# Kernel tuning notes

Measured on AMD Instinct MI355X. Metric: run time of the kernel, lower is better.

The kernel has to match this reference:

```python
import jax, jax.numpy as jnp
import numpy as np

# Model dims (match init_kwargs defaults)
H, DK, DV = 6, 256, 512          # num_heads, head_k_dim, head_v_dim (= head_dim*expand_v)
HID = 2048                       # hidden_size
CONV = 4                         # short conv kernel size
NORM_EPS = 1e-5


def causal_dwconv_silu(x, w):
    """Depthwise causal conv1d (kernel CONV) + SiLU. x: [B,T,C], w: [C,K]."""
    K = w.shape[1]
    xp = jnp.pad(x, ((0, 0), (K - 1, 0), (0, 0)))
    y = jax.lax.conv_general_dilated(
        jnp.transpose(xp, (0, 2, 1)),            # [B,C,T+K-1]
        w[:, None, :],                            # [C,1,K] depthwise
        (1,), 'VALID', feature_group_count=w.shape[0])
    return jax.nn.silu(jnp.transpose(y, (0, 2, 1)))  # [B,T,C]


def l2norm(x, eps=1e-6):
    return x * jax.lax.rsqrt(jnp.sum(x * x, axis=-1, keepdims=True) + eps)


def setup_inputs() -> dict:
    key = jax.random.key(0)
    ks = jax.random.split(key, 16)
    B, T = 2, 4096
    s = HID ** -0.5
    return dict(
        hidden_states=jax.random.normal(ks[0], (B, T, HID), jnp.float32),
        Wq=jax.random.normal(ks[1], (H * DK, HID), jnp.float32) * s,
        Wk=jax.random.normal(ks[2], (H * DK, HID), jnp.float32) * s,
        Wv=jax.random.normal(ks[3], (H * DV, HID), jnp.float32) * s,
        Wb=jax.random.normal(ks[4], (H, HID), jnp.float32) * s,
        Wa=jax.random.normal(ks[5], (H, HID), jnp.float32) * s,
        A_log=jnp.log(jax.random.uniform(ks[6], (H,), jnp.float32, 0.5, 16.0)),
        dt_bias=jax.random.normal(ks[7], (H,), jnp.float32) * 0.1,
        conv_wq=jax.random.normal(ks[8], (H * DK, CONV), jnp.float32) * 0.5,
        conv_wk=jax.random.normal(ks[9], (H * DK, CONV), jnp.float32) * 0.5,
        conv_wv=jax.random.normal(ks[10], (H * DV, CONV), jnp.float32) * 0.5,
        Wg=jax.random.normal(ks[11], (H * DV, HID), jnp.float32) * s,
        norm_w=jnp.ones((DV,), jnp.float32),
        Wo=jax.random.normal(ks[12], (HID, H * DV), jnp.float32) * (H * DV) ** -0.5,
    )


def reference(hidden_states, Wq, Wk, Wv, Wb, Wa, A_log, dt_bias,
              conv_wq, conv_wk, conv_wv, Wg, norm_w, Wo):
    x = hidden_states
    B, T, _ = x.shape
    # projections + short conv + SiLU
    q = causal_dwconv_silu(x @ Wq.T, conv_wq).reshape(B, T, H, DK)
    k = causal_dwconv_silu(x @ Wk.T, conv_wk).reshape(B, T, H, DK)
    v = causal_dwconv_silu(x @ Wv.T, conv_wv).reshape(B, T, H, DV)
    beta = jax.nn.sigmoid(x @ Wb.T)                                   # [B,T,H]
    g = -jnp.exp(A_log) * jax.nn.softplus(x @ Wa.T + dt_bias)        # [B,T,H] (log decay)
    # qk l2-norm + scale, as in gated delta rule kernels
    q = l2norm(q) * (DK ** -0.5)
    k = l2norm(k)

    # gated delta rule recurrence: S_t = exp(g_t)*S_{t-1} + beta_t * k_t (v_t - k_t^T exp(g_t) S_{t-1})
    def step(S, inp):
        qt, kt, vt, gt, bt = inp  # [B,H,DK],[B,H,DK],[B,H,DV],[B,H],[B,H]
        S = S * jnp.exp(gt)[..., None, None]                  # [B,H,DK,DV]
        v_new = vt - jnp.einsum('bhk,bhkv->bhv', kt, S)
        S = S + bt[..., None, None] * (kt[..., :, None] * v_new[..., None, :])
        o = jnp.einsum('bhk,bhkv->bhv', qt, S)
        return S, o

    S0 = jnp.zeros((B, H, DK, DV), x.dtype)
    tm = lambda a: jnp.moveaxis(a, 1, 0)  # time-major for scan
    _, o = jax.lax.scan(step, S0, (tm(q), tm(k), tm(v), tm(g), tm(beta)))
    o = jnp.moveaxis(o, 0, 1)  # [B,T,H,DV]

    # per-head RMSNorm (fp32 var) then SiLU output gate
    var = jnp.mean(jnp.square(o.astype(jnp.float32)), axis=-1, keepdims=True)
    o = o * jax.lax.rsqrt(var + NORM_EPS).astype(o.dtype) * norm_w
    gate = (x @ Wg.T).reshape(B, T, H, DV)
    o = o * jax.nn.silu(gate)
    return o.reshape(B, T, H * DV) @ Wo.T
```

## Files before the change

kernel.cpp:

```cpp
#include <hip/hip_runtime.h>
#include <hip/hip_bf16.h>
#include <math.h>

#define NH 6
#define DKk 256
#define DVv 512
#define HIDDIM 2048
#define TT 4096
#define NBb 2
#define MTOK (NBb*TT)
#define CH 64
#define NCH (TT/CH)
#define SCLN 136

typedef __hip_bfloat16 bf16;
typedef __attribute__((ext_vector_type(8))) short bf16x8;
typedef __attribute__((ext_vector_type(4))) float f32x4;

union FragU { bf16x8 v; uint2 u2[2]; uint4 u4; };
union BfBits { bf16 h; unsigned short s; };
union U4S8 { uint4 u; unsigned short s[8]; };

__device__ inline float bflo(unsigned u) { return __uint_as_float(u << 16); }
__device__ inline float bfhi(unsigned u) { return __uint_as_float(u & 0xffff0000u); }
__device__ inline unsigned short bfbits(float f) {
    BfBits b; b.h = __float2bfloat16(f); return b.s;
}
__device__ inline float bf2f(unsigned short s) { return __uint_as_float(((unsigned)s) << 16); }
__device__ inline uint4 pack8(float4 a, float4 b) {
    U4S8 r;
    r.s[0] = bfbits(a.x); r.s[1] = bfbits(a.y); r.s[2] = bfbits(a.z); r.s[3] = bfbits(a.w);
    r.s[4] = bfbits(b.x); r.s[5] = bfbits(b.y); r.s[6] = bfbits(b.z); r.s[7] = bfbits(b.w);
    return r.u;
}
__device__ inline uint2 packh4(float a, float b, float c, float d) {
    union { unsigned short s[4]; uint2 u; } r;
    r.s[0] = bfbits(a); r.s[1] = bfbits(b); r.s[2] = bfbits(c); r.s[3] = bfbits(d);
    return r.u;
}
__device__ inline bf16x8 pk8t(f32x4 a, f32x4 b) {
    U4S8 r;
    r.s[0] = bfbits(a[0]); r.s[1] = bfbits(a[1]); r.s[2] = bfbits(a[2]); r.s[3] = bfbits(a[3]);
    r.s[4] = bfbits(b[0]); r.s[5] = bfbits(b[1]); r.s[6] = bfbits(b[2]); r.s[7] = bfbits(b[3]);
    FragU f; f.u4 = r.u; return f.v;
}

typedef const __attribute__((address_space(1))) void* gas_ptr;
typedef __attribute__((address_space(3))) void* las_ptr;
__device__ inline void gld16(const void* g, void* s) {
    __builtin_amdgcn_global_load_lds((gas_ptr)g, (las_ptr)s, 16, 0, 0);
}

__device__ inline bf16x8 lfrag256(const short* sh, int n0, int k0) {
    int lane = threadIdx.x & 63;
    int r = n0 + (lane & 15);
    int c = k0 + ((lane >> 4) * 4);
    FragU f;
    f.u2[0] = *(const uint2*)((const char*)sh + (((r * 256 + c) * 2) ^ ((r & 7) << 4)));
    f.u2[1] = *(const uint2*)((const char*)sh + (((r * 256 + c + 16) * 2) ^ ((r & 7) << 4)));
    return f.v;
}
__device__ inline bf16x8 lfrag64(const short* sh, int n0, int k0) {
    int lane = threadIdx.x & 63;
    int r = n0 + (lane & 15);
    int c = k0 + ((lane >> 4) * 4);
    FragU f;
    f.u2[0] = *(const uint2*)((const char*)sh + (((r * 64 + c) * 2) ^ ((r & 7) << 4)));
    f.u2[1] = *(const uint2*)((const char*)sh + (((r * 64 + c + 16) * 2) ^ ((r & 7) << 4)));
    return f.v;
}
__device__ inline bf16x8 lfrag72(const short* sh, int n0, int k0) {
    int lane = threadIdx.x & 63;
    int r = n0 + (lane & 15);
    int c = k0 + ((lane >> 4) * 4);
    FragU f;
    f.u2[0] = *(const uint2*)((const char*)sh + (r * 72 + c) * 2);
    f.u2[1] = *(const uint2*)((const char*)sh + (r * 72 + c + 16) * 2);
    return f.v;
}
__device__ inline bf16x8 mfrag(const float* Msh, const float* colscale, int m0, int k0) {
    int lane = threadIdx.x & 63;
    int t = m0 + (lane & 15);
    int s0 = k0 + ((lane >> 4) * 4);
    U4S8 r;
#pragma unroll
    for (int i = 0; i < 4; ++i) {
        r.s[i]     = bfbits(Msh[t * 68 + s0 + i]      * colscale[s0 + i]);
        r.s[4 + i] = bfbits(Msh[t * 68 + s0 + 16 + i] * colscale[s0 + 16 + i]);
    }
    FragU f; f.u4 = r.u; return f.v;
}

__global__ __launch_bounds__(256) void cvt_bf16(const float* __restrict__ in,
                                                bf16* __restrict__ out, int n) {
    for (int i = (blockIdx.x * 256 + threadIdx.x) * 4; i < n; i += gridDim.x * 256 * 4) {
        float4 v = *(const float4*)(in + i);
        *(uint2*)(out + i) = packh4(v.x, v.y, v.z, v.w);
    }
}

template <typename TC>
__global__ __launch_bounds__(256) void mfma_gemm_bb(const bf16* __restrict__ A,
                                                    const bf16* __restrict__ B,
                                                    TC* __restrict__ C,
                                                    int M, int N, int K) {
    __shared__ __align__(16) short As[128 * 64];
    __shared__ __align__(16) short Bs[128 * 64];
    const int tid = threadIdx.x;
    const int lane = tid & 63;
    const int wid = tid >> 6;
    const int wr = wid >> 1, wc = wid & 1;
    const int bm = blockIdx.y * 128, bn = blockIdx.x * 128;

    f32x4 acc[4][4];
#pragma unroll
    for (int i = 0; i < 4; ++i)
#pragma unroll
        for (int j = 0; j < 4; ++j) acc[i][j] = f32x4{0.f, 0.f, 0.f, 0.f};

    for (int k0 = 0; k0 < K; k0 += 64) {
        __syncthreads();
#pragma unroll
        for (int i = 0; i < 4; ++i) {
            int r0 = wid * 32 + i * 8;
            const bf16* ga = A + (size_t)(bm + r0 + (lane >> 3)) * K + k0 + (lane & 7) * 8;
            const bf16* gb = B + (size_t)(bn + r0 + (lane >> 3)) * K + k0 + (lane & 7) * 8;
            gld16(ga, &As[r0 * 64]);
            gld16(gb, &Bs[r0 * 64]);
        }
        __syncthreads();
#pragma unroll
        for (int kk = 0; kk < 2; ++kk) {
            bf16x8 af[4], bfr[4];
#pragma unroll
            for (int i = 0; i < 4; ++i) {
                FragU f;
                f.u4 = *(const uint4*)&As[(wr * 64 + i * 16 + (lane & 15)) * 64 +
                                          kk * 32 + (lane >> 4) * 8];
                af[i] = f.v;
            }
#pragma unroll
            for (int j = 0; j < 4; ++j) {
                FragU f;
                f.u4 = *(const uint4*)&Bs[(wc * 64 + j * 16 + (lane & 15)) * 64 +
                                          kk * 32 + (lane >> 4) * 8];
                bfr[j] = f.v;
            }
#pragma unroll
            for (int i = 0; i < 4; ++i)
#pragma unroll
                for (int j = 0; j < 4; ++j)
                    acc[i][j] = __builtin_amdgcn_mfma_f32_16x16x32_bf16(
                        af[i], bfr[j], acc[i][j], 0, 0, 0);
        }
    }
#pragma unroll
    for (int i = 0; i < 4; ++i)
#pragma unroll
        for (int j = 0; j < 4; ++j) {
            int row = bm + wr * 64 + i * 16 + (lane >> 4) * 4;
            int col = bn + wc * 64 + j * 16 + (lane & 15);
#pragma unroll
            for (int qi = 0; qi < 4; ++qi) {
                float vv = acc[i][j][qi];
                if constexpr (sizeof(TC) == 2)
                    C[(size_t)(row + qi) * N + col] = __float2bfloat16(vv);
                else
                    C[(size_t)(row + qi) * N + col] = vv;
            }
        }
}

template <typename TA, typename TC>
__global__ __launch_bounds__(256) void mfma_gemm_nt(const TA* __restrict__ A,
                                                    const float* __restrict__ B,
                                                    TC* __restrict__ C,
                                                    int M, int N, int K) {
    __shared__ __align__(16) short As[128 * 64];
    __shared__ __align__(16) short Bs[128 * 64];
    const int tid = threadIdx.x;
    const int lane = tid & 63;
    const int wid = tid >> 6;
    const int wr = wid >> 1, wc = wid & 1;
    const int bm = blockIdx.y * 128, bn = blockIdx.x * 128;
    const int srow = tid >> 1;
    const int sks = (tid & 1) * 32;

    f32x4 acc[4][4];
#pragma unroll
    for (int i = 0; i < 4; ++i)
#pragma unroll
        for (int j = 0; j < 4; ++j) acc[i][j] = f32x4{0.f, 0.f, 0.f, 0.f};

    auto swzb = [](int row, int kelem) {
        return ((row * 64 + kelem) * 2) ^ ((row & 7) << 4);
    };
    uint4 ra[4], rb[4];
    auto fetch = [&](int k0) {
        if constexpr (sizeof(TA) == 2) {
            const uint4* pa = (const uint4*)(A + (size_t)(bm + srow) * K + k0 + sks);
#pragma unroll
            for (int j = 0; j < 4; ++j) ra[j] = pa[j];
        } else {
            const float4* pa = (const float4*)(A + (size_t)(bm + srow) * K + k0 + sks);
#pragma unroll
            for (int j = 0; j < 4; ++j) ra[j] = pack8(pa[2 * j], pa[2 * j + 1]);
        }
        const float4* pb = (const float4*)(B + (size_t)(bn + srow) * K + k0 + sks);
#pragma unroll
        for (int j = 0; j < 4; ++j) rb[j] = pack8(pb[2 * j], pb[2 * j + 1]);
    };
    auto store_lds = [&]() {
#pragma unroll
        for (int j = 0; j < 4; ++j) {
            int byte = swzb(srow, sks + 8 * j);
            *(uint4*)((char*)As + byte) = ra[j];
            *(uint4*)((char*)Bs + byte) = rb[j];
        }
    };
    auto rdfrag = [&](const short* Sm, int row, int kbase) {
        FragU f;
        int ko = kbase + (lane >> 4) * 4;
        f.u2[0] = *(const uint2*)((const char*)Sm + swzb(row, ko));
        f.u2[1] = *(const uint2*)((const char*)Sm + swzb(row, ko + 16));
        return f.v;
    };

    fetch(0);
    for (int k0 = 0; k0 < K; k0 += 64) {
        __syncthreads();
        store_lds();
        __syncthreads();
        if (k0 + 64 < K) fetch(k0 + 64);
#pragma unroll
        for (int kk = 0; kk < 2; ++kk) {
            bf16x8 af[4], bfr[4];
#pragma unroll
            for (int i = 0; i < 4; ++i)
                af[i] = rdfrag(As, wr * 64 + i * 16 + (lane & 15), kk * 32);
#pragma unroll
            for (int j = 0; j < 4; ++j)
                bfr[j] = rdfrag(Bs, wc * 64 + j * 16 + (lane & 15), kk * 32);
#pragma unroll
            for (int i = 0; i < 4; ++i)
#pragma unroll
                for (int j = 0; j < 4; ++j)
                    acc[i][j] = __builtin_amdgcn_mfma_f32_16x16x32_bf16(
                        af[i], bfr[j], acc[i][j], 0, 0, 0);
        }
    }
#pragma unroll
    for (int i = 0; i < 4; ++i)
#pragma unroll
        for (int j = 0; j < 4; ++j) {
            int row = bm + wr * 64 + i * 16 + (lane >> 4) * 4;
            int col = bn + wc * 64 + j * 16 + (lane & 15);
#pragma unroll
            for (int qi = 0; qi < 4; ++qi) {
                float vv = acc[i][j][qi];
                if constexpr (sizeof(TC) == 2)
                    C[(size_t)(row + qi) * N + col] = __float2bfloat16(vv);
                else
                    C[(size_t)(row + qi) * N + col] = vv;
            }
        }
}

__global__ __launch_bounds__(256) void convnorm_qk(const bf16* __restrict__ pre,
                                                   const float* __restrict__ cw,
                                                   bf16* __restrict__ out,
                                                   float scale) {
    const int bth = blockIdx.x;
    const int h = bth % NH;
    const int bt = bth / NH;
    const int t = bt % TT;
    const int d = threadIdx.x;
    const int c = h * DKk + d;
    const int C = NH * DKk;
    const bf16* p = pre + (size_t)bt * C + c;

    float w0 = cw[c * 4 + 0], w1 = cw[c * 4 + 1], w2 = cw[c * 4 + 2], w3 = cw[c * 4 + 3];
    float y = w3 * __bfloat162float(p[0]);
    if (t >= 1) y = fmaf(w2, __bfloat162float(p[-(ptrdiff_t)C]), y);
    if (t >= 2) y = fmaf(w1, __bfloat162float(p[-(ptrdiff_t)(2 * C)]), y);
    if (t >= 3) y = fmaf(w0, __bfloat162float(p[-(ptrdiff_t)(3 * C)]), y);
    y = y / (1.f + expf(-y));

    float s = y * y;
#pragma unroll
    for (int off = 32; off >= 1; off >>= 1) s += __shfl_down(s, off, 64);
    __shared__ float red[4];
    if ((threadIdx.x & 63) == 0) red[threadIdx.x >> 6] = s;
    __syncthreads();
    float tot = (red[0] + red[1]) + (red[2] + red[3]);
    out[(size_t)bt * C + c] = __float2bfloat16(y * rsqrtf(tot + 1e-6f) * scale);
}

__global__ __launch_bounds__(256) void conv_v_kernel(const bf16* __restrict__ pre,
                                                     const float* __restrict__ cw,
                                                     bf16* __restrict__ out) {
    const int C = NH * DVv;
    int idx = blockIdx.x * 256 + threadIdx.x;
    int c = idx % C;
    int bt = idx / C;
    int t = bt % TT;
    const bf16* p = pre + (size_t)bt * C + c;
    float y = cw[c * 4 + 3] * __bfloat162float(p[0]);
    if (t >= 1) y = fmaf(cw[c * 4 + 2], __bfloat162float(p[-(ptrdiff_t)C]), y);
    if (t >= 2) y = fmaf(cw[c * 4 + 1], __bfloat162float(p[-(ptrdiff_t)(2 * C)]), y);
    if (t >= 3) y = fmaf(cw[c * 4 + 0], __bfloat162float(p[-(ptrdiff_t)(3 * C)]), y);
    out[(size_t)bt * C + c] = __float2bfloat16(y / (1.f + expf(-y)));
}

__global__ __launch_bounds__(256) void proj_ab(const float* __restrict__ x,
                                               const float* __restrict__ Wb,
                                               const float* __restrict__ Wa,
                                               const float* __restrict__ A_log,
                                               const float* __restrict__ dt_bias,
                                               float* __restrict__ beta,
                                               float* __restrict__ g) {
    const int bt = blockIdx.x;
    const int tid = threadIdx.x;
    const float* xr = x + (size_t)bt * HIDDIM;
    float accb[NH], acca[NH];
#pragma unroll
    for (int h = 0; h < NH; ++h) { accb[h] = 0.f; acca[h] = 0.f; }
    for (int k0 = tid; k0 < HIDDIM; k0 += 256) {
        float xv = xr[k0];
#pragma unroll
        for (int h = 0; h < NH; ++h) {
            accb[h] = fmaf(xv, Wb[h * HIDDIM + k0], accb[h]);
            acca[h] = fmaf(xv, Wa[h * HIDDIM + k0], acca[h]);
        }
    }
#pragma unroll
    for (int h = 0; h < NH; ++h) {
#pragma unroll
        for (int off = 32; off >= 1; off >>= 1) {
            accb[h] += __shfl_down(accb[h], off, 64);
            acca[h] += __shfl_down(acca[h], off, 64);
        }
    }
    __shared__ float redb[NH][4], reda[NH][4];
    int wv = tid >> 6;
    if ((tid & 63) == 0) {
#pragma unroll
        for (int h = 0; h < NH; ++h) { redb[h][wv] = accb[h]; reda[h][wv] = acca[h]; }
    }
    __syncthreads();
    if (tid < NH) {
        float sb = (redb[tid][0] + redb[tid][1]) + (redb[tid][2] + redb[tid][3]);
        float sa = (reda[tid][0] + reda[tid][1]) + (reda[tid][2] + reda[tid][3]);
        beta[(size_t)bt * NH + tid] = 1.f / (1.f + expf(-sb));
        float xg = sa + dt_bias[tid];
        float sp = fmaxf(xg, 0.f) + log1pf(expf(-fabsf(xg)));
        g[(size_t)bt * NH + tid] = -expf(A_log[tid]) * sp;
    }
}

__global__ __launch_bounds__(256) void chunk_prep(const bf16* __restrict__ qbuf,
                                                  const bf16* __restrict__ kbuf,
                                                  bf16* __restrict__ vbuf,
                                                  bf16* __restrict__ tvbuf,
                                                  const float* __restrict__ gbuf,
                                                  const float* __restrict__ bbuf,
                                                  bf16* __restrict__ Bmat,
                                                  float* __restrict__ scl) {
    __shared__ __align__(16) short Ksh[64 * 256];
    __shared__ __align__(16) short Qsh[64 * 256];
    __shared__ __align__(16) float Ash[64 * 68];
    __shared__ __align__(16) short Vt[128 * 72];
    __shared__ float Lsh[64], betash[64], lamsh[64], blamsh[64];

    const int blk = blockIdx.x;
    const int c = blk % NCH;
    const int hh = (blk / NCH) % NH;
    const int b = blk / (NCH * NH);
    const int tid = threadIdx.x;
    const int wid = tid >> 6;
    const int lane = tid & 63;
    const int bt0 = b * TT + c * CH;
    const int cid = (b * NH + hh) * NCH + c;

    {
        int r = tid >> 2, c0 = (tid & 3) * 64;
        const uint4* kg = (const uint4*)(kbuf + (size_t)(bt0 + r) * 1536 + hh * 256 + c0);
        const uint4* qg = (const uint4*)(qbuf + (size_t)(bt0 + r) * 1536 + hh * 256 + c0);
#pragma unroll
        for (int j = 0; j < 8; ++j) {
            int byte = ((r * 256 + c0 + j * 8) * 2) ^ ((r & 7) << 4);
            *(uint4*)((char*)Ksh + byte) = kg[j];
            *(uint4*)((char*)Qsh + byte) = qg[j];
        }
    }
    if (tid < 64) {
        float gv = gbuf[(size_t)(bt0 + tid) * NH + hh];
        float bv = bbuf[(size_t)(bt0 + tid) * NH + hh];
        float L = gv;
#pragma unroll
        for (int off = 1; off < 64; off <<= 1) {
            float o = __shfl_up(L, off, 64);
            if (lane >= off) L += o;
        }
        float L63 = __shfl(L, 63, 64);
        float lam = expf(L);
        Lsh[tid] = L; betash[tid] = bv; lamsh[tid] = lam; blamsh[tid] = bv * lam;
        scl[(size_t)cid * SCLN + tid] = expf(L63 - L);
        scl[(size_t)cid * SCLN + 68 + tid] = lam;
        if (tid == 63) scl[(size_t)cid * SCLN + 64] = lam;
    }
    __syncthreads();

    f32x4 akk[4], aqk[4];
#pragma unroll
    for (int n = 0; n < 4; ++n) { akk[n] = f32x4{0,0,0,0}; aqk[n] = f32x4{0,0,0,0}; }
#pragma unroll
    for (int kk = 0; kk < 8; ++kk) {
        bf16x8 aK = lfrag256(Ksh, wid * 16, kk * 32);
        bf16x8 aQ = lfrag256(Qsh, wid * 16, kk * 32);
#pragma unroll
        for (int n = 0; n < 4; ++n) {
            bf16x8 bK = lfrag256(Ksh, n * 16, kk * 32);
            akk[n] = __builtin_amdgcn_mfma_f32_16x16x32_bf16(aK, bK, akk[n], 0, 0, 0);
            aqk[n] = __builtin_amdgcn_mfma_f32_16x16x32_bf16(aQ, bK, aqk[n], 0, 0, 0);
        }
    }
#pragma unroll
    for (int n = 0; n < 4; ++n)
#pragma unroll
        for (int qi = 0; qi < 4; ++qi) {
            int i = wid * 16 + (lane >> 4) * 4 + qi;
            int s = n * 16 + (lane & 15);
            float av = 0.f, bvv = 0.f;
            if (s <= i) {
                float sc2 = expf(Lsh[i] - Lsh[s]);
                if (s < i) av = betash[i] * sc2 * akk[n][qi];
                bvv = sc2 * aqk[n][qi];
            }
            Ash[i * 68 + s] = av;
            Bmat[(size_t)cid * 4096 + i * 64 + s] = __float2bfloat16(bvv);
        }
    __syncthreads();

    if (wid == 0) {
        float mm[64];
        mm[0] = (lane == 0) ? 1.f : 0.f;
#pragma unroll
        for (int t = 1; t < 64; ++t) {
            float a0 = 0.f, a1 = 0.f, a2 = 0.f, a3 = 0.f;
#pragma unroll
            for (int s = 0; s < t; ++s) {
                float Av = Ash[t * 68 + s];
                if ((s & 3) == 0) a0 = fmaf(Av, mm[s], a0);
                else if ((s & 3) == 1) a1 = fmaf(Av, mm[s], a1);
                else if ((s & 3) == 2) a2 = fmaf(Av, mm[s], a2);
                else a3 = fmaf(Av, mm[s], a3);
            }
            mm[t] = ((t == lane) ? 1.f : 0.f) - ((a0 + a1) + (a2 + a3));
        }
#pragma unroll
        for (int t = 0; t < 64; ++t) Ash[t * 68 + lane] = mm[t];
    }
    __syncthreads();

    for (int q = 0; q < 4; ++q) {
        {
            int i = tid >> 2, d0 = (tid & 3) * 32;
            const uint4* vg = (const uint4*)(vbuf + (size_t)(bt0 + i) * 3072 + hh * 512 + q * 128 + d0);
#pragma unroll
            for (int jb = 0; jb < 4; ++jb) {
                U4S8 u; u.u = vg[jb];
#pragma unroll
                for (int e = 0; e < 8; ++e)
                    Vt[(d0 + jb * 8 + e) * 72 + i] = (short)u.s[e];
            }
        }
        __syncthreads();
        f32x4 acc[8];
#pragma unroll
        for (int n = 0; n < 8; ++n) acc[n] = f32x4{0,0,0,0};
#pragma unroll
        for (int kk = 0; kk < 2; ++kk) {
            bf16x8 am = mfrag(Ash, betash, wid * 16, kk * 32);
#pragma unroll
            for (int n = 0; n < 8; ++n) {
                bf16x8 bv8 = lfrag72(Vt, n * 16, kk * 32);
                acc[n] = __builtin_amdgcn_mfma_f32_16x16x32_bf16(am, bv8, acc[n], 0, 0, 0);
            }
        }
#pragma unroll
        for (int n = 0; n < 8; ++n)
#pragma unroll
            for (int qi = 0; qi < 4; ++qi) {
                int t = wid * 16 + (lane >> 4) * 4 + qi;
                int d = q * 128 + n * 16 + (lane & 15);
                tvbuf[(size_t)(bt0 + t) * 3072 + hh * 512 + d] = __float2bfloat16(acc[n][qi]);
            }
        __syncthreads();
    }

    {
        int j = tid;
        unsigned short rowv[64];
#pragma unroll
        for (int s = 0; s < 64; ++s)
            rowv[s] = *(const unsigned short*)((const char*)Ksh + (((s * 256 + j) * 2) ^ ((s & 7) << 4)));
#pragma unroll
        for (int sb = 0; sb < 8; ++sb) {
            U4S8 u;
#pragma unroll
            for (int e = 0; e < 8; ++e) u.s[e] = rowv[sb * 8 + e];
            *(uint4*)((char*)Qsh + (((j * 64 + sb * 8) * 2) ^ ((j & 7) << 4))) = u.u;
        }
    }
    __syncthreads();

    {
        f32x4 acc[16];
#pragma unroll
        for (int n = 0; n < 16; ++n) acc[n] = f32x4{0,0,0,0};
#pragma unroll
        for (int kk = 0; kk < 2; ++kk) {
            bf16x8 am = mfrag(Ash, blamsh, wid * 16, kk * 32);
#pragma unroll
            for (int n = 0; n < 16; ++n) {
                bf16x8 bk = lfrag64(Qsh, n * 16, kk * 32);
                acc[n] = __builtin_amdgcn_mfma_f32_16x16x32_bf16(am, bk, acc[n], 0, 0, 0);
            }
        }
#pragma unroll
        for (int n = 0; n < 16; ++n)
#pragma unroll
            for (int qi = 0; qi < 4; ++qi) {
                int t = wid * 16 + (lane >> 4) * 4 + qi;
                int j = n * 16 + (lane & 15);
                vbuf[(size_t)(bt0 + t) * 3072 + hh * 512 + j] = __float2bfloat16(acc[n][qi]);
            }
    }
    {
        int j = tid;
#pragma unroll
        for (int sb = 0; sb < 8; ++sb) {
            uint4 u = *(uint4*)((char*)Qsh + (((j * 64 + sb * 8) * 2) ^ ((j & 7) << 4)));
            *(uint4*)(vbuf + (size_t)(bt0 + (j >> 2)) * 3072 + hh * 512 + 256 + (j & 3) * 64 + sb * 8) = u;
        }
    }
}

__global__ __launch_bounds__(512, 1) void chunk_scan3(const bf16* __restrict__ qbuf,
                                                      const bf16* __restrict__ vbuf,
                                                      bf16* __restrict__ tvbuf,
                                                      const bf16* __restrict__ Bmat,
                                                      const float* __restrict__ scl) {
    __shared__ __align__(16) short TkL[64 * 256];
    __shared__ __align__(16) short QL[64 * 256];
    __shared__ __align__(16) short KTL[256 * 64];
    __shared__ __align__(16) short BmL[64 * 64];
    const int tid = threadIdx.x;
    const int wid = tid >> 6;
    const int lane = tid & 63;
    const int part = blockIdx.x & 3;
    const int bh = blockIdx.x >> 2;
    const int hh = bh % NH;
    const int b = bh / NH;
    const int slice = part * 8 + wid;
    const int dglob0 = hh * 512 + slice * 16;
    const int tlo = (lane >> 4) * 4;
    const int dcol = lane & 15;

    f32x4 S[16];
#pragma unroll
    for (int i = 0; i < 16; ++i) S[i] = f32x4{0.f, 0.f, 0.f, 0.f};

    for (int c = 0; c < NCH; ++c) {
        const int bt0 = b * TT + c * CH;
        const int cid = (b * NH + hh) * NCH + c;
        const float* sc = scl + (size_t)cid * SCLN;
        const float lamC = sc[64];

        __syncthreads();
        {
            int r = tid >> 3;
            int bc0 = (tid & 7) * 16;
#pragma unroll
            for (int rd = 0; rd < 4; ++rd) {
                int bc = bc0 + rd * 128;
                uint4 tv = *(const uint4*)((const char*)(vbuf) +
                    ((size_t)(bt0 + r) * 3072 + hh * 512) * 2 + bc);
                uint4 qv = *(const uint4*)((const char*)(qbuf) +
                    ((size_t)(bt0 + r) * 1536 + hh * 256) * 2 + bc);
                int byte = (r * 512 + bc) ^ ((r & 7) << 4);
                *(uint4*)((char*)TkL + byte) = tv;
                *(uint4*)((char*)QL + byte) = qv;
            }
        }
        {
            int j = tid >> 1;
            int bc0 = (tid & 1) * 16;
#pragma unroll
            for (int rd = 0; rd < 4; ++rd) {
                int bc = bc0 + rd * 32;
                uint4 v = *(const uint4*)((const char*)(vbuf) +
                    ((size_t)(bt0 + (j >> 2)) * 3072 + hh * 512 + 256 + (j & 3) * 64) * 2 + bc);
                int byte = (j * 128 + bc) ^ ((j & 7) << 4);
                *(uint4*)((char*)KTL + byte) = v;
            }
        }
        {
            int r = tid >> 3;
            int bc = (tid & 7) * 16;
            uint4 v = *(const uint4*)((const char*)(Bmat) +
                ((size_t)cid * 4096 + r * 64) * 2 + bc);
            int byte = (r * 128 + bc) ^ ((r & 7) << 4);
            *(uint4*)((char*)BmL + byte) = v;
        }
        __syncthreads();

        bf16x8 sfr[8];
#pragma unroll
        for (int kk = 0; kk < 8; ++kk) sfr[kk] = pk8t(S[2 * kk], S[2 * kk + 1]);

        f32x4 P[4], O[4];
#pragma unroll
        for (int tf = 0; tf < 4; ++tf) { P[tf] = f32x4{0,0,0,0}; O[tf] = f32x4{0,0,0,0}; }
#pragma unroll
        for (int tf = 0; tf < 4; ++tf)
#pragma unroll
            for (int kk = 0; kk < 8; ++kk) {
                bf16x8 aT = lfrag256(TkL, tf * 16, kk * 32);
                bf16x8 aQ = lfrag256(QL, tf * 16, kk * 32);
                P[tf] = __builtin_amdgcn_mfma_f32_16x16x32_bf16(aT, sfr[kk], P[tf], 0, 0, 0);
                O[tf] = __builtin_amdgcn_mfma_f32_16x16x32_bf16(aQ, sfr[kk], O[tf], 0, 0, 0);
            }
#pragma unroll
        for (int tf = 0; tf < 4; ++tf) {
            float4 lam4 = *(const float4*)(sc + 68 + tf * 16 + tlo);
            O[tf][0] *= lam4.x; O[tf][1] *= lam4.y; O[tf][2] *= lam4.z; O[tf][3] *= lam4.w;
            int t = tf * 16 + tlo;
#pragma unroll
            for (int qi = 0; qi < 4; ++qi) {
                float tv = __bfloat162float(tvbuf[(size_t)(bt0 + t + qi) * 3072 + dglob0 + dcol]);
                P[tf][qi] = tv - P[tf][qi];
            }
        }
        bf16x8 ufr0 = pk8t(P[0], P[1]);
        bf16x8 ufr1 = pk8t(P[2], P[3]);
#pragma unroll
        for (int tf = 0; tf < 4; ++tf) {
            bf16x8 aB0 = lfrag64(BmL, tf * 16, 0);
            bf16x8 aB1 = lfrag64(BmL, tf * 16, 32);
            O[tf] = __builtin_amdgcn_mfma_f32_16x16x32_bf16(aB0, ufr0, O[tf], 0, 0, 0);
            O[tf] = __builtin_amdgcn_mfma_f32_16x16x32_bf16(aB1, ufr1, O[tf], 0, 0, 0);
            int t = tf * 16 + tlo;
#pragma unroll
            for (int qi = 0; qi < 4; ++qi)
                tvbuf[(size_t)(bt0 + t + qi) * 3072 + dglob0 + dcol] = __float2bfloat16(O[tf][qi]);
        }
        bf16x8 utfr[2];
#pragma unroll
        for (int k2 = 0; k2 < 2; ++k2) {
            float4 e0 = *(const float4*)(sc + k2 * 32 + tlo);
            float4 e1 = *(const float4*)(sc + k2 * 32 + 16 + tlo);
            f32x4 ua = P[2 * k2], ub = P[2 * k2 + 1];
            ua[0] *= e0.x; ua[1] *= e0.y; ua[2] *= e0.z; ua[3] *= e0.w;
            ub[0] *= e1.x; ub[1] *= e1.y; ub[2] *= e1.z; ub[3] *= e1.w;
            utfr[k2] = pk8t(ua, ub);
        }
#pragma unroll
        for (int kt = 0; kt < 16; ++kt) {
            S[kt][0] *= lamC; S[kt][1] *= lamC; S[kt][2] *= lamC; S[kt][3] *= lamC;
        }
#pragma unroll
        for (int kt = 0; kt < 16; ++kt)
#pragma unroll
            for (int k2 = 0; k2 < 2; ++k2) {
                bf16x8 aK = lfrag64(KTL, kt * 16, k2 * 32);
                S[kt] = __builtin_amdgcn_mfma_f32_16x16x32_bf16(aK, utfr[k2], S[kt], 0, 0, 0);
            }
    }
}

__global__ __launch_bounds__(256) void rmsgate_kernel(bf16* __restrict__ o,
                                                      const bf16* __restrict__ gate,
                                                      const float* __restrict__ norm_w) {
    const int bhead = blockIdx.x;
    const int d = threadIdx.x;
    bf16* op = o + (size_t)bhead * DVv;
    const bf16* gp = gate + (size_t)bhead * DVv;
    float x0 = __bfloat162float(op[d]), x1 = __bfloat162float(op[d + 256]);
    float s = x0 * x0 + x1 * x1;
#pragma unroll
    for (int off = 32; off >= 1; off >>= 1) s += __shfl_down(s, off, 64);
    __shared__ float red[4];
    if ((threadIdx.x & 63) == 0) red[threadIdx.x >> 6] = s;
    __syncthreads();
    float tot = (red[0] + red[1]) + (red[2] + red[3]);
    float r = rsqrtf(tot * (1.f / DVv) + 1e-5f);
    float g0 = __bfloat162float(gp[d]), g1 = __bfloat162float(gp[d + 256]);
    g0 = g0 / (1.f + expf(-g0));
    g1 = g1 / (1.f + expf(-g1));
    op[d]       = __float2bfloat16(x0 * r * norm_w[d] * g0);
    op[d + 256] = __float2bfloat16(x1 * r * norm_w[d + 256] * g1);
}

__global__ void fill_kernel(float* p, int n, float v) {
    int i = blockIdx.x * 256 + threadIdx.x;
    if (i < n) p[i] = v;
}

extern "C" void kernel_launch(void* const* d_in, const int* in_sizes, int n_in,
                              void* d_out, int out_size, void* d_ws, size_t ws_size,
                              hipStream_t stream) {
    const float* x       = (const float*)d_in[0];
    const float* Wq      = (const float*)d_in[1];
    const float* Wk      = (const float*)d_in[2];
    const float* Wv      = (const float*)d_in[3];
    const float* Wb      = (const float*)d_in[4];
    const float* Wa      = (const float*)d_in[5];
    const float* A_log   = (const float*)d_in[6];
    const float* dt_bias = (const float*)d_in[7];
    const float* cwq     = (const float*)d_in[8];
    const float* cwk     = (const float*)d_in[9];
    const float* cwv     = (const float*)d_in[10];
    const float* Wg      = (const float*)d_in[11];
    const float* norm_w  = (const float*)d_in[12];
    const float* Wo      = (const float*)d_in[13];
    float* out = (float*)d_out;

    bf16* qb = (bf16*)d_out;
    bf16* kb = qb + (size_t)MTOK * 1536;

    const size_t elemsA = (size_t)MTOK * 3072;
    const size_t elemsB = (size_t)MTOK * 3072;
    bf16* wsA   = (bf16*)d_ws;
    bf16* wsB   = wsA + elemsA;
    bf16* Bmat  = wsB + elemsB;
    float* scl  = (float*)(Bmat + (size_t)NBb * NH * NCH * 4096);
    float* betab = scl + (size_t)NBb * NH * NCH * SCLN;
    float* gb    = betab + (size_t)MTOK * NH;
    size_t need_base = ((size_t)(gb - (float*)d_ws) + (size_t)MTOK * NH) * sizeof(float);
    bf16* xb    = (bf16*)(gb + (size_t)MTOK * NH);
    bf16* Wslot = xb + (size_t)MTOK * HIDDIM;
    size_t need_fast = need_base +
        ((size_t)MTOK * HIDDIM + (size_t)3072 * HIDDIM) * sizeof(bf16);

    if (ws_size < need_base) {
        fill_kernel<<<(out_size + 255) / 256, 256, 0, stream>>>(out, out_size, 1e9f);
        return;
    }

    dim3 blk(256);
    const bool fast = (ws_size >= need_fast);

    if (fast) {
        cvt_bf16<<<2048, blk, 0, stream>>>(x, xb, MTOK * HIDDIM);
        cvt_bf16<<<1024, blk, 0, stream>>>(Wq, Wslot, 1536 * HIDDIM);
        mfma_gemm_bb<bf16><<<dim3(12, 64), blk, 0, stream>>>(xb, Wslot, wsA, MTOK, 1536, HIDDIM);
        convnorm_qk<<<MTOK * NH, dim3(DKk), 0, stream>>>(wsA, cwq, qb, 0.0625f);
        cvt_bf16<<<1024, blk, 0, stream>>>(Wk, Wslot, 1536 * HIDDIM);
        mfma_gemm_bb<bf16><<<dim3(12, 64), blk, 0, stream>>>(xb, Wslot, wsA, MTOK, 1536, HIDDIM);
        convnorm_qk<<<MTOK * NH, dim3(DKk), 0, stream>>>(wsA, cwk, kb, 1.0f);
        cvt_bf16<<<2048, blk, 0, stream>>>(Wv, Wslot, 3072 * HIDDIM);
        mfma_gemm_bb<bf16><<<dim3(24, 64), blk, 0, stream>>>(xb, Wslot, wsB, MTOK, 3072, HIDDIM);
        conv_v_kernel<<<(MTOK * 3072) / 256, blk, 0, stream>>>(wsB, cwv, wsA);
        proj_ab<<<MTOK, blk, 0, stream>>>(x, Wb, Wa, A_log, dt_bias, betab, gb);
        chunk_prep<<<NBb * NH * NCH, blk, 0, stream>>>(qb, kb, wsA, wsB, gb, betab, Bmat, scl);
        chunk_scan3<<<NBb * NH * 4, dim3(512), 0, stream>>>(qb, wsA, wsB, Bmat, scl);
        cvt_bf16<<<2048, blk, 0, stream>>>(Wg, Wslot, 3072 * HIDDIM);
        mfma_gemm_bb<bf16><<<dim3(24, 64), blk, 0, stream>>>(xb, Wslot, wsA, MTOK, 3072, HIDDIM);
        rmsgate_kernel<<<MTOK * NH, blk, 0, stream>>>(wsB, wsA, norm_w);
        cvt_bf16<<<2048, blk, 0, stream>>>(Wo, Wslot, 2048 * 3072);
        mfma_gemm_bb<float><<<dim3(16, 64), blk, 0, stream>>>(wsB, Wslot, out, MTOK, 2048, 3072);
    } else {
        mfma_gemm_nt<float, bf16><<<dim3(12, 64), blk, 0, stream>>>(x, Wq, wsA, MTOK, 1536, HIDDIM);
        convnorm_qk<<<MTOK * NH, dim3(DKk), 0, stream>>>(wsA, cwq, qb, 0.0625f);
        mfma_gemm_nt<float, bf16><<<dim3(12, 64), blk, 0, stream>>>(x, Wk, wsA, MTOK, 1536, HIDDIM);
        convnorm_qk<<<MTOK * NH, dim3(DKk), 0, stream>>>(wsA, cwk, kb, 1.0f);
        mfma_gemm_nt<float, bf16><<<dim3(24, 64), blk, 0, stream>>>(x, Wv, wsB, MTOK, 3072, HIDDIM);
        conv_v_kernel<<<(MTOK * 3072) / 256, blk, 0, stream>>>(wsB, cwv, wsA);
        proj_ab<<<MTOK, blk, 0, stream>>>(x, Wb, Wa, A_log, dt_bias, betab, gb);
        chunk_prep<<<NBb * NH * NCH, blk, 0, stream>>>(qb, kb, wsA, wsB, gb, betab, Bmat, scl);
        chunk_scan3<<<NBb * NH * 4, dim3(512), 0, stream>>>(qb, wsA, wsB, Bmat, scl);
        mfma_gemm_nt<float, bf16><<<dim3(24, 64), blk, 0, stream>>>(x, Wg, wsA, MTOK, 3072, HIDDIM);
        rmsgate_kernel<<<MTOK * NH, blk, 0, stream>>>(wsB, wsA, norm_w);
        mfma_gemm_nt<bf16, float><<<dim3(16, 64), blk, 0, stream>>>(wsB, Wo, out, MTOK, 2048, 3072);
    }
}
```

Baseline: 1.848 ms.

## Merge chunk-scan work into two 1024-thread blocks per batch-head

The chunked delta-rule scan now runs as two 1024-thread blocks per (batch, head), each owning 16 value-column slices, instead of four 512-thread blocks with 8 slices each. Each block still loads the shared per-chunk tiles (T/k, q, k-transposed and the B matrix), so this halves the redundant global-to-LDS staging per head, with 1024 threads cooperating on every load. In exchange the grid shrinks from 48 to 24 blocks, barriers span 16 waves, and the launch bound of 1024 threads halves the registers available per wave. That could cause the 64-register state accumulator to spill.

```diff
diff --git a/kernel.cpp b/kernel.cpp
--- a/kernel.cpp
+++ b/kernel.cpp
@@ -547,11 +547,11 @@
     }
 }
 
-__global__ __launch_bounds__(512, 1) void chunk_scan3(const bf16* __restrict__ qbuf,
-                                                      const bf16* __restrict__ vbuf,
-                                                      bf16* __restrict__ tvbuf,
-                                                      const bf16* __restrict__ Bmat,
-                                                      const float* __restrict__ scl) {
+__global__ __launch_bounds__(1024, 4) void chunk_scan6(const bf16* __restrict__ qbuf,
+                                                       const bf16* __restrict__ vbuf,
+                                                       bf16* __restrict__ tvbuf,
+                                                       const bf16* __restrict__ Bmat,
+                                                       const float* __restrict__ scl) {
     __shared__ __align__(16) short TkL[64 * 256];
     __shared__ __align__(16) short QL[64 * 256];
     __shared__ __align__(16) short KTL[256 * 64];
@@ -559,11 +559,11 @@
     const int tid = threadIdx.x;
     const int wid = tid >> 6;
     const int lane = tid & 63;
-    const int part = blockIdx.x & 3;
-    const int bh = blockIdx.x >> 2;
+    const int half = blockIdx.x & 1;
+    const int bh = blockIdx.x >> 1;
     const int hh = bh % NH;
     const int b = bh / NH;
-    const int slice = part * 8 + wid;
+    const int slice = half * 16 + wid;
     const int dglob0 = hh * 512 + slice * 16;
     const int tlo = (lane >> 4) * 4;
     const int dcol = lane & 15;
@@ -579,34 +579,30 @@
         const float lamC = sc[64];
 
         __syncthreads();
-        {
-            int r = tid >> 3;
-            int bc0 = (tid & 7) * 16;
-#pragma unroll
-            for (int rd = 0; rd < 4; ++rd) {
-                int bc = bc0 + rd * 128;
-                uint4 tv = *(const uint4*)((const char*)(vbuf) +
-                    ((size_t)(bt0 + r) * 3072 + hh * 512) * 2 + bc);
-                uint4 qv = *(const uint4*)((const char*)(qbuf) +
-                    ((size_t)(bt0 + r) * 1536 + hh * 256) * 2 + bc);
-                int byte = (r * 512 + bc) ^ ((r & 7) << 4);
-                *(uint4*)((char*)TkL + byte) = tv;
-                *(uint4*)((char*)QL + byte) = qv;
-            }
-        }
-        {
-            int j = tid >> 1;
-            int bc0 = (tid & 1) * 16;
-#pragma unroll
-            for (int rd = 0; rd < 4; ++rd) {
-                int bc = bc0 + rd * 32;
-                uint4 v = *(const uint4*)((const char*)(vbuf) +
-                    ((size_t)(bt0 + (j >> 2)) * 3072 + hh * 512 + 256 + (j & 3) * 64) * 2 + bc);
-                int byte = (j * 128 + bc) ^ ((j & 7) << 4);
-                *(uint4*)((char*)KTL + byte) = v;
-            }
-        }
-        {
+#pragma unroll
+        for (int it = 0; it < 2; ++it) {
+            int u = it * 1024 + tid;
+            int r = u >> 5;
+            int bc = (u & 31) * 16;
+            uint4 tv = *(const uint4*)((const char*)(vbuf) +
+                ((size_t)(bt0 + r) * 3072 + hh * 512) * 2 + bc);
+            uint4 qv = *(const uint4*)((const char*)(qbuf) +
+                ((size_t)(bt0 + r) * 1536 + hh * 256) * 2 + bc);
+            int byte = (r * 512 + bc) ^ ((r & 7) << 4);
+            *(uint4*)((char*)TkL + byte) = tv;
+            *(uint4*)((char*)QL + byte) = qv;
+        }
+#pragma unroll
+        for (int it = 0; it < 2; ++it) {
+            int u = it * 1024 + tid;
+            int j = u >> 3;
+            int bc = (u & 7) * 16;
+            uint4 v = *(const uint4*)((const char*)(vbuf) +
+                ((size_t)(bt0 + (j >> 2)) * 3072 + hh * 512 + 256 + (j & 3) * 64) * 2 + bc);
+            int byte = (j * 128 + bc) ^ ((j & 7) << 4);
+            *(uint4*)((char*)KTL + byte) = v;
+        }
+        if (tid < 512) {
             int r = tid >> 3;
             int bc = (tid & 7) * 16;
             uint4 v = *(const uint4*)((const char*)(Bmat) +
@@ -765,7 +761,7 @@
         conv_v_kernel<<<(MTOK * 3072) / 256, blk, 0, stream>>>(wsB, cwv, wsA);
         proj_ab<<<MTOK, blk, 0, stream>>>(x, Wb, Wa, A_log, dt_bias, betab, gb);
         chunk_prep<<<NBb * NH * NCH, blk, 0, stream>>>(qb, kb, wsA, wsB, gb, betab, Bmat, scl);
-        chunk_scan3<<<NBb * NH * 4, dim3(512), 0, stream>>>(qb, wsA, wsB, Bmat, scl);
+        chunk_scan6<<<NBb * NH * 2, dim3(1024), 0, stream>>>(qb, wsA, wsB, Bmat, scl);
         cvt_bf16<<<2048, blk, 0, stream>>>(Wg, Wslot, 3072 * HIDDIM);
         mfma_gemm_bb<bf16><<<dim3(24, 64), blk, 0, stream>>>(xb, Wslot, wsA, MTOK, 3072, HIDDIM);
         rmsgate_kernel<<<MTOK * NH, blk, 0, stream>>>(wsB, wsA, norm_w);
@@ -780,7 +776,7 @@
         conv_v_kernel<<<(MTOK * 3072) / 256, blk, 0, stream>>>(wsB, cwv, wsA);
         proj_ab<<<MTOK, blk, 0, stream>>>(x, Wb, Wa, A_log, dt_bias, betab, gb);
         chunk_prep<<<NBb * NH * NCH, blk, 0, stream>>>(qb, kb, wsA, wsB, gb, betab, Bmat, scl);
-        chunk_scan3<<<NBb * NH * 4, dim3(512), 0, stream>>>(qb, wsA, wsB, Bmat, scl);
+        chunk_scan6<<<NBb * NH * 2, dim3(1024), 0, stream>>>(qb, wsA, wsB, Bmat, scl);
         mfma_gemm_nt<float, bf16><<<dim3(24, 64), blk, 0, stream>>>(x, Wg, wsA, MTOK, 3072, HIDDIM);
         rmsgate_kernel<<<MTOK * NH, blk, 0, stream>>>(wsB, wsA, norm_w);
         mfma_gemm_nt<bf16, float><<<dim3(16, 64), blk, 0, stream>>>(wsB, Wo, out, MTOK, 2048, 3072);
```

New measurement: 2.573 ms. 39.2% more time.

## Double-buffer chunk scan staging with async global-to-LDS loads

Applied to the files above, without the earlier changes.

The sequential chunk-scan kernel now prefetches the next chunk's Tk and Q tiles into a double-buffered LDS region using global_load_lds, so the loads overlap with the current chunk's MFMA work. The KT tile is staged asynchronously too. The B matrix fragments are read straight from global memory instead of through LDS. The aim is to hide the per-chunk global load latency on the serial critical path, at the cost of more LDS and reordered barriers, with some risk of a synchronization hazard on the KT buffer.

```diff
diff --git a/kernel.cpp b/kernel.cpp
--- a/kernel.cpp
+++ b/kernel.cpp
@@ -51,6 +51,12 @@
     __builtin_amdgcn_global_load_lds((gas_ptr)g, (las_ptr)s, 16, 0, 0);
 }
 
+__device__ inline bf16x8 gfrag(const bf16* base, size_t stride, int n0, int k0) {
+    int lane = threadIdx.x & 63;
+    const bf16* p = base + (size_t)(n0 + (lane & 15)) * stride + k0 + ((lane >> 4) * 4);
+    FragU f; f.u2[0] = *(const uint2*)p; f.u2[1] = *(const uint2*)(p + 16);
+    return f.v;
+}
 __device__ inline bf16x8 lfrag256(const short* sh, int n0, int k0) {
     int lane = threadIdx.x & 63;
     int r = n0 + (lane & 15);
@@ -58,6 +64,15 @@
     FragU f;
     f.u2[0] = *(const uint2*)((const char*)sh + (((r * 256 + c) * 2) ^ ((r & 7) << 4)));
     f.u2[1] = *(const uint2*)((const char*)sh + (((r * 256 + c + 16) * 2) ^ ((r & 7) << 4)));
+    return f.v;
+}
+__device__ inline bf16x8 lfrag512(const short* sh, int n0, int k0, int cofs) {
+    int lane = threadIdx.x & 63;
+    int r = n0 + (lane & 15);
+    int c = cofs + k0 + ((lane >> 4) * 4);
+    FragU f;
+    f.u2[0] = *(const uint2*)((const char*)sh + (((r * 512 + c) * 2) ^ ((r & 7) << 4)));
+    f.u2[1] = *(const uint2*)((const char*)sh + (((r * 512 + c + 16) * 2) ^ ((r & 7) << 4)));
     return f.v;
 }
 __device__ inline bf16x8 lfrag64(const short* sh, int n0, int k0) {
@@ -547,15 +562,13 @@
     }
 }
 
-__global__ __launch_bounds__(512, 1) void chunk_scan3(const bf16* __restrict__ qbuf,
+__global__ __launch_bounds__(512, 1) void chunk_scan7(const bf16* __restrict__ qbuf,
                                                       const bf16* __restrict__ vbuf,
                                                       bf16* __restrict__ tvbuf,
                                                       const bf16* __restrict__ Bmat,
                                                       const float* __restrict__ scl) {
-    __shared__ __align__(16) short TkL[64 * 256];
-    __shared__ __align__(16) short QL[64 * 256];
+    __shared__ __align__(16) short TQ[2][64 * 512];
     __shared__ __align__(16) short KTL[256 * 64];
-    __shared__ __align__(16) short BmL[64 * 64];
     const int tid = threadIdx.x;
     const int wid = tid >> 6;
     const int lane = tid & 63;
@@ -568,53 +581,52 @@
     const int tlo = (lane >> 4) * 4;
     const int dcol = lane & 15;
 
+    auto stage_TkQ = [&](int c2, int bufi) {
+        if (c2 < NCH) {
+            const int bt = b * TT + c2 * CH;
+            short* dst = TQ[bufi];
+#pragma unroll
+            for (int i = 0; i < 8; ++i) {
+                int r = wid * 8 + i;
+                int u = lane ^ (r & 7);
+                const char* src;
+                if (u < 32)
+                    src = (const char*)(vbuf + (size_t)(bt + r) * 3072 + hh * 512) + u * 16;
+                else
+                    src = (const char*)(qbuf + (size_t)(bt + r) * 1536 + hh * 256) + (u - 32) * 16;
+                gld16(src, &dst[r * 512]);
+            }
+        }
+    };
+    auto stage_KT = [&](int c2) {
+        const int bt = b * TT + c2 * CH;
+#pragma unroll
+        for (int i = 0; i < 4; ++i) {
+            int j0 = (wid * 4 + i) * 8;
+            int j = j0 + (lane >> 3);
+            int u = (lane & 7) ^ (j & 7);
+            const char* src = (const char*)(vbuf + (size_t)(bt + (j >> 2)) * 3072 +
+                                            hh * 512 + 256 + (j & 3) * 64) + u * 16;
+            gld16(src, &KTL[j0 * 64]);
+        }
+    };
+
     f32x4 S[16];
 #pragma unroll
     for (int i = 0; i < 16; ++i) S[i] = f32x4{0.f, 0.f, 0.f, 0.f};
+
+    stage_TkQ(0, 0);
+    __syncthreads();
 
     for (int c = 0; c < NCH; ++c) {
         const int bt0 = b * TT + c * CH;
         const int cid = (b * NH + hh) * NCH + c;
         const float* sc = scl + (size_t)cid * SCLN;
         const float lamC = sc[64];
-
-        __syncthreads();
-        {
-            int r = tid >> 3;
-            int bc0 = (tid & 7) * 16;
-#pragma unroll
-            for (int rd = 0; rd < 4; ++rd) {
-                int bc = bc0 + rd * 128;
-                uint4 tv = *(const uint4*)((const char*)(vbuf) +
-                    ((size_t)(bt0 + r) * 3072 + hh * 512) * 2 + bc);
-                uint4 qv = *(const uint4*)((const char*)(qbuf) +
-                    ((size_t)(bt0 + r) * 1536 + hh * 256) * 2 + bc);
-                int byte = (r * 512 + bc) ^ ((r & 7) << 4);
-                *(uint4*)((char*)TkL + byte) = tv;
-                *(uint4*)((char*)QL + byte) = qv;
-            }
-        }
-        {
-            int j = tid >> 1;
-            int bc0 = (tid & 1) * 16;
-#pragma unroll
-            for (int rd = 0; rd < 4; ++rd) {
-                int bc = bc0 + rd * 32;
-                uint4 v = *(const uint4*)((const char*)(vbuf) +
-                    ((size_t)(bt0 + (j >> 2)) * 3072 + hh * 512 + 256 + (j & 3) * 64) * 2 + bc);
-                int byte = (j * 128 + bc) ^ ((j & 7) << 4);
-                *(uint4*)((char*)KTL + byte) = v;
-            }
-        }
-        {
-            int r = tid >> 3;
-            int bc = (tid & 7) * 16;
-            uint4 v = *(const uint4*)((const char*)(Bmat) +
-                ((size_t)cid * 4096 + r * 64) * 2 + bc);
-            int byte = (r * 128 + bc) ^ ((r & 7) << 4);
-            *(uint4*)((char*)BmL + byte) = v;
-        }
-        __syncthreads();
+        const short* buf = TQ[c & 1];
+
+        stage_TkQ(c + 1, (c + 1) & 1);
+        stage_KT(c);
 
         bf16x8 sfr[8];
 #pragma unroll
@@ -627,8 +639,8 @@
         for (int tf = 0; tf < 4; ++tf)
 #pragma unroll
             for (int kk = 0; kk < 8; ++kk) {
-                bf16x8 aT = lfrag256(TkL, tf * 16, kk * 32);
-                bf16x8 aQ = lfrag256(QL, tf * 16, kk * 32);
+                bf16x8 aT = lfrag512(buf, tf * 16, kk * 32, 0);
+                bf16x8 aQ = lfrag512(buf, tf * 16, kk * 32, 256);
                 P[tf] = __builtin_amdgcn_mfma_f32_16x16x32_bf16(aT, sfr[kk], P[tf], 0, 0, 0);
                 O[tf] = __builtin_amdgcn_mfma_f32_16x16x32_bf16(aQ, sfr[kk], O[tf], 0, 0, 0);
             }
@@ -647,8 +659,8 @@
         bf16x8 ufr1 = pk8t(P[2], P[3]);
 #pragma unroll
         for (int tf = 0; tf < 4; ++tf) {
-            bf16x8 aB0 = lfrag64(BmL, tf * 16, 0);
-            bf16x8 aB1 = lfrag64(BmL, tf * 16, 32);
+            bf16x8 aB0 = gfrag(Bmat + (size_t)cid * 4096, 64, tf * 16, 0);
+            bf16x8 aB1 = gfrag(Bmat + (size_t)cid * 4096, 64, tf * 16, 32);
             O[tf] = __builtin_amdgcn_mfma_f32_16x16x32_bf16(aB0, ufr0, O[tf], 0, 0, 0);
             O[tf] = __builtin_amdgcn_mfma_f32_16x16x32_bf16(aB1, ufr1, O[tf], 0, 0, 0);
             int t = tf * 16 + tlo;
@@ -666,6 +678,9 @@
             ub[0] *= e1.x; ub[1] *= e1.y; ub[2] *= e1.z; ub[3] *= e1.w;
             utfr[k2] = pk8t(ua, ub);
         }
+
+        __syncthreads();
+
 #pragma unroll
         for (int kt = 0; kt < 16; ++kt) {
             S[kt][0] *= lamC; S[kt][1] *= lamC; S[kt][2] *= lamC; S[kt][3] *= lamC;
@@ -677,6 +692,8 @@
                 bf16x8 aK = lfrag64(KTL, kt * 16, k2 * 32);
                 S[kt] = __builtin_amdgcn_mfma_f32_16x16x32_bf16(aK, utfr[k2], S[kt], 0, 0, 0);
             }
+
+        __syncthreads();
     }
 }
 
@@ -765,7 +782,7 @@
         conv_v_kernel<<<(MTOK * 3072) / 256, blk, 0, stream>>>(wsB, cwv, wsA);
         proj_ab<<<MTOK, blk, 0, stream>>>(x, Wb, Wa, A_log, dt_bias, betab, gb);
         chunk_prep<<<NBb * NH * NCH, blk, 0, stream>>>(qb, kb, wsA, wsB, gb, betab, Bmat, scl);
-        chunk_scan3<<<NBb * NH * 4, dim3(512), 0, stream>>>(qb, wsA, wsB, Bmat, scl);
+        chunk_scan7<<<NBb * NH * 4, dim3(512), 0, stream>>>(qb, wsA, wsB, Bmat, scl);
         cvt_bf16<<<2048, blk, 0, stream>>>(Wg, Wslot, 3072 * HIDDIM);
         mfma_gemm_bb<bf16><<<dim3(24, 64), blk, 0, stream>>>(xb, Wslot, wsA, MTOK, 3072, HIDDIM);
         rmsgate_kernel<<<MTOK * NH, blk, 0, stream>>>(wsB, wsA, norm_w);
@@ -780,7 +797,7 @@
         conv_v_kernel<<<(MTOK * 3072) / 256, blk, 0, stream>>>(wsB, cwv, wsA);
         proj_ab<<<MTOK, blk, 0, stream>>>(x, Wb, Wa, A_log, dt_bias, betab, gb);
         chunk_prep<<<NBb * NH * NCH, blk, 0, stream>>>(qb, kb, wsA, wsB, gb, betab, Bmat, scl);
-        chunk_scan3<<<NBb * NH * 4, dim3(512), 0, stream>>>(qb, wsA, wsB, Bmat, scl);
+        chunk_scan7<<<NBb * NH * 4, dim3(512), 0, stream>>>(qb, wsA, wsB, Bmat, scl);
         mfma_gemm_nt<float, bf16><<<dim3(24, 64), blk, 0, stream>>>(x, Wg, wsA, MTOK, 3072, HIDDIM);
         rmsgate_kernel<<<MTOK * NH, blk, 0, stream>>>(wsB, wsA, norm_w);
         mfma_gemm_nt<bf16, float><<<dim3(16, 64), blk, 0, stream>>>(wsB, Wo, out, MTOK, 2048, 3072);
```

New measurement: 2.298 ms. 24.3% more time.
